# Performance work log

Measured on AMD Instinct MI355X. Metric: run time of the kernel, lower is better.

Reference implementation:

```python
import jax, jax.numpy as jnp
import numpy as np

N_HEADS = 12
EPS = 1e-6
H_DIM = 768


def setup_inputs() -> dict:
    key = jax.random.key(0)
    ks = jax.random.split(key, 10)
    B, M, T, C = 2, 64, 512, H_DIM
    x = jax.random.normal(ks[0], (B, M, T, C), dtype=jnp.float32)
    mask = jnp.ones((B, M, T), dtype=jnp.float32)
    s = 1.0 / np.sqrt(C)
    Wq = jax.random.normal(ks[1], (C, C), dtype=jnp.float32) * s
    bq = jax.random.normal(ks[2], (C,), dtype=jnp.float32) * 0.01
    Wk = jax.random.normal(ks[3], (C, C), dtype=jnp.float32) * s
    bk = jax.random.normal(ks[4], (C,), dtype=jnp.float32) * 0.01
    Wv = jax.random.normal(ks[5], (C, C), dtype=jnp.float32) * s
    bv = jax.random.normal(ks[6], (C,), dtype=jnp.float32) * 0.01
    Wp = jax.random.normal(ks[7], (C, C), dtype=jnp.float32) * s
    bp = jax.random.normal(ks[8], (C,), dtype=jnp.float32) * 0.01
    return {"x": x, "mask": mask, "Wq": Wq, "bq": bq, "Wk": Wk, "bk": bk,
            "Wv": Wv, "bv": bv, "Wp": Wp, "bp": bp}


def reference(x, mask, Wq, bq, Wk, bk, Wv, bv, Wp, bp):
    B, M, T, C = x.shape
    N, D = N_HEADS, C // N_HEADS
    # projections: nn.Linear -> x @ W.T + b, then [B,M,T,N,D] -> [B,M,N,T,D]
    q = (x @ Wq.T + bq).reshape(B, M, T, N, D).transpose(0, 1, 3, 2, 4)
    k = (x @ Wk.T + bk).reshape(B, M, T, N, D).transpose(0, 1, 3, 2, 4)
    v = (x @ Wv.T + bv).reshape(B, M, T, N, D).transpose(0, 1, 3, 2, 4)
    q = jax.nn.elu(q) + 1.0
    k = jax.nn.elu(k) + 1.0
    k = k * mask[:, :, None, :, None]
    # KtV[b,m,n,d,e] = sum_t k[b,m,n,t,d] * v[b,m,n,t,e]   (small [D,D] per head)
    KtV = jnp.einsum('bmntd,bmnte->bmnde', k, v)
    # Z[b,m,n,t] = 1 / (q . sum_t' k + eps)
    Z = 1.0 / (jnp.einsum('bmntd,bmnd->bmnt', q, k.sum(axis=-2)) + EPS)
    # torch code does Z.expand(...,T,D) @ KtV, which equals Z * KtV.sum(over d)
    S = KtV.sum(axis=-2)                       # [B,M,N,E]
    V = Z[..., None] * S[:, :, :, None, :]     # [B,M,N,T,E]
    V = V.transpose(0, 1, 3, 2, 4).reshape(B, M, T, N * D)
    out = V @ Wp.T + bp
    return out
```

## Files before the change

### kernel.cpp

```cpp
#include <hip/hip_runtime.h>
#include <hip/hip_bf16.h>
#include <stdint.h>

typedef short short8 __attribute__((ext_vector_type(8)));
typedef float f32x4 __attribute__((ext_vector_type(4)));

#define EPS_Z 1e-6f

__device__ __forceinline__ unsigned short f2bf(float f) {
  uint32_t b = __float_as_uint(f);
  b += 0x7FFFu + ((b >> 16) & 1u);
  return (unsigned short)(b >> 16);
}
__device__ __forceinline__ float bf2f(unsigned short u) {
  return __uint_as_float(((uint32_t)u) << 16);
}

__device__ __forceinline__ void gl16(const unsigned short* g, unsigned short* l) {
  __builtin_amdgcn_global_load_lds(
      (const __attribute__((address_space(1))) unsigned int*)g,
      (__attribute__((address_space(3))) unsigned int*)l, 16, 0, 0);
}

__global__ __launch_bounds__(256) void k_cvt(const float* __restrict__ in,
                                             unsigned short* __restrict__ out, int n) {
  int i = (blockIdx.x * 256 + threadIdx.x) * 8;
  if (i >= n) return;
  float4 a = *(const float4*)(in + i);
  float4 b = *(const float4*)(in + i + 4);
  union { unsigned short u[8]; short8 v; } r;
  r.u[0] = f2bf(a.x); r.u[1] = f2bf(a.y); r.u[2] = f2bf(a.z); r.u[3] = f2bf(a.w);
  r.u[4] = f2bf(b.x); r.u[5] = f2bf(b.y); r.u[6] = f2bf(b.z); r.u[7] = f2bf(b.w);
  *(short8*)(out + i) = r.v;
}

__global__ __launch_bounds__(512, 2) void k_projqk(
    const unsigned short* __restrict__ xbf,
    const unsigned short* __restrict__ Wkbf,
    const unsigned short* __restrict__ Wqbf,
    const float* __restrict__ bk,
    const float* __restrict__ bq,
    const float* __restrict__ mask,
    float* __restrict__ kd,
    float* __restrict__ ksum_part,
    unsigned short* __restrict__ qbf)
{
  __shared__ unsigned short Ab[128][64];
  __shared__ unsigned short Bkb[128][64];
  __shared__ unsigned short Bqb[128][64];
  __shared__ float rowf[128];
  __shared__ float kcol[2][128];

  const int tid = threadIdx.x;
  const int lane = tid & 63;
  const int wid = tid >> 6;
  const int isQ = wid >> 2;
  const int w2 = wid & 3;
  const int wr = w2 >> 1, wc = w2 & 1;
  const int colTile = blockIdx.x;
  const int rowTile = blockIdx.y;
  const int bm = rowTile >> 2;
  const int trow = rowTile & 3;
  const size_t rowBase = (size_t)rowTile * 128;
  const int colBase = colTile * 128;
  const int lrow = lane & 15;
  const int lgrp = lane >> 4;

  if (tid < 128) rowf[tid] = mask[bm * 512 + trow * 128 + tid];

  f32x4 acc[4][4] = {};

  for (int kt = 0; kt < 12; ++kt) {
    const int k0 = kt * 64;
    __syncthreads();
#pragma unroll
    for (int c = 0; c < 2; ++c) {
      const int chunk = c * 512 + tid;
      const int r = chunk >> 3;
      const int cc = chunk & 7;
      const int scc = cc ^ (r & 7);
      const int ldst = c * 4096 + wid * 512;
      gl16(xbf + (rowBase + r) * 768 + k0 + scc * 8, &Ab[0][0] + ldst);
      gl16(Wkbf + (size_t)(colBase + r) * 768 + k0 + scc * 8, &Bkb[0][0] + ldst);
      gl16(Wqbf + (size_t)(colBase + r) * 768 + k0 + scc * 8, &Bqb[0][0] + ldst);
    }
    __syncthreads();
    const unsigned short* Bsel = isQ ? &Bqb[0][0] : &Bkb[0][0];
#pragma unroll
    for (int kk = 0; kk < 64; kk += 32) {
      short8 av[4], bv4[4];
#pragma unroll
      for (int rf = 0; rf < 4; ++rf) {
        const int row = wr * 64 + rf * 16 + lrow;
        const int cidx = ((kk >> 3) + lgrp) ^ (row & 7);
        av[rf] = *(const short8*)&Ab[row][cidx * 8];
      }
#pragma unroll
      for (int cf = 0; cf < 4; ++cf) {
        const int row = wc * 64 + cf * 16 + lrow;
        const int cidx = ((kk >> 3) + lgrp) ^ (row & 7);
        bv4[cf] = *(const short8*)(Bsel + row * 64 + cidx * 8);
      }
#pragma unroll
      for (int rf = 0; rf < 4; ++rf)
#pragma unroll
        for (int cf = 0; cf < 4; ++cf)
          acc[rf][cf] = __builtin_amdgcn_mfma_f32_16x16x32_bf16(
              av[rf], bv4[cf], acc[rf][cf], 0, 0, 0);
    }
  }

  const float* bias = isQ ? bq : bk;
  float bvv[4];
#pragma unroll
  for (int cf = 0; cf < 4; ++cf)
    bvv[cf] = bias[colBase + wc * 64 + cf * 16 + lrow];
#pragma unroll
  for (int rf = 0; rf < 4; ++rf)
#pragma unroll
    for (int cf = 0; cf < 4; ++cf)
#pragma unroll
      for (int j = 0; j < 4; ++j) {
        float v = acc[rf][cf][j] + bvv[cf];
        v = (v > 0.0f) ? (v + 1.0f) : __expf(v);
        if (!isQ) v *= rowf[wr * 64 + rf * 16 + lgrp * 4 + j];
        acc[rf][cf][j] = v;
      }

  const int head = colTile * 2 + wc;

  if (!isQ) {
#pragma unroll
    for (int rf = 0; rf < 4; ++rf)
#pragma unroll
      for (int j = 0; j < 4; ++j) {
        float s = acc[rf][0][j] + acc[rf][1][j] + acc[rf][2][j] + acc[rf][3][j];
        s += __shfl_xor(s, 1, 64);
        s += __shfl_xor(s, 2, 64);
        s += __shfl_xor(s, 4, 64);
        s += __shfl_xor(s, 8, 64);
        if ((lane & 15) == 0) {
          const int t = trow * 128 + wr * 64 + rf * 16 + lgrp * 4 + j;
          kd[((size_t)bm * 512 + t) * 12 + head] = s;
        }
      }
#pragma unroll
    for (int cf = 0; cf < 4; ++cf) {
      float s = 0.f;
#pragma unroll
      for (int rf = 0; rf < 4; ++rf)
#pragma unroll
        for (int j = 0; j < 4; ++j) s += acc[rf][cf][j];
      s += __shfl_xor(s, 16, 64);
      s += __shfl_xor(s, 32, 64);
      if (lane < 16) kcol[wr][wc * 64 + cf * 16 + lane] = s;
    }
  } else {
#pragma unroll
    for (int rf = 0; rf < 4; ++rf)
#pragma unroll
      for (int j = 0; j < 4; ++j) {
        const int t = trow * 128 + wr * 64 + rf * 16 + lgrp * 4 + j;
        unsigned short* qp = qbf + (((size_t)bm * 12 + head) * 512 + t) * 64 + lrow;
#pragma unroll
        for (int cf = 0; cf < 4; ++cf)
          qp[cf * 16] = f2bf(acc[rf][cf][j]);
      }
  }

  __syncthreads();
  if (tid < 128)
    ksum_part[((size_t)bm * 4 + trow) * 768 + colBase + tid] =
        kcol[0][tid] + kcol[1][tid];
}

__global__ __launch_bounds__(192) void k_xk(const unsigned short* __restrict__ xbf,
                                            const float* __restrict__ kd,
                                            float* __restrict__ xk_part) {
  __shared__ float kdl[128][12];
  const int bm = blockIdx.x, ts = blockIdx.y, tid = threadIdx.x;
  for (int i = tid; i < 128 * 12; i += 192)
    kdl[i / 12][i % 12] = kd[((size_t)bm * 512 + ts * 128 + i / 12) * 12 + (i % 12)];
  __syncthreads();
  float a[12][4];
#pragma unroll
  for (int n = 0; n < 12; ++n)
#pragma unroll
    for (int j = 0; j < 4; ++j) a[n][j] = 0.f;
  const int c = tid * 4;
  const unsigned short* xp = xbf + ((size_t)bm * 512 + ts * 128) * 768 + c;
  for (int t = 0; t < 128; ++t) {
    ushort4 xv = *(const ushort4*)(xp + (size_t)t * 768);
    const float x0 = bf2f(xv.x), x1 = bf2f(xv.y), x2 = bf2f(xv.z), x3 = bf2f(xv.w);
#pragma unroll
    for (int n = 0; n < 12; ++n) {
      const float kv = kdl[t][n];
      a[n][0] += kv * x0; a[n][1] += kv * x1; a[n][2] += kv * x2; a[n][3] += kv * x3;
    }
  }
  float* op = xk_part + ((size_t)bm * 4 + ts) * 12 * 768 + c;
#pragma unroll
  for (int n = 0; n < 12; ++n)
    *(float4*)(op + (size_t)n * 768) = make_float4(a[n][0], a[n][1], a[n][2], a[n][3]);
}

__global__ __launch_bounds__(256) void k_sg(const float* __restrict__ ksum_part,
                                            const float* __restrict__ xk_part,
                                            const float* __restrict__ Wv,
                                            const float* __restrict__ bv,
                                            const float* __restrict__ Wp,
                                            float* __restrict__ G) {
  __shared__ __align__(16) float xk_l[768];
  __shared__ __align__(16) float S_l[64];
  __shared__ float kdsum_s;
  const int bm = blockIdx.x, n = blockIdx.y, tid = threadIdx.x;

  if (tid < 192) {
    const float* xp = xk_part + (size_t)bm * 4 * 9216 + n * 768 + tid * 4;
    float4 a = *(const float4*)(xp);
    float4 b = *(const float4*)(xp + 9216);
    float4 c = *(const float4*)(xp + 18432);
    float4 d = *(const float4*)(xp + 27648);
    *(float4*)&xk_l[tid * 4] = make_float4(a.x + b.x + c.x + d.x,
                                           a.y + b.y + c.y + d.y,
                                           a.z + b.z + c.z + d.z,
                                           a.w + b.w + c.w + d.w);
  } else {
    const int d = tid - 192;
    const float* kp = ksum_part + (size_t)bm * 4 * 768 + n * 64 + d;
    float s = kp[0] + kp[768] + kp[1536] + kp[2304];
    s += __shfl_xor(s, 1, 64);
    s += __shfl_xor(s, 2, 64);
    s += __shfl_xor(s, 4, 64);
    s += __shfl_xor(s, 8, 64);
    s += __shfl_xor(s, 16, 64);
    s += __shfl_xor(s, 32, 64);
    if (d == 0) kdsum_s = s;
  }
  __syncthreads();

  {
    const int e = tid >> 2, q = tid & 3;
    const float4* wv = (const float4*)(Wv + (size_t)(n * 64 + e) * 768 + q * 192);
    const float4* xp4 = (const float4*)(xk_l + q * 192);
    float s = 0.f;
#pragma unroll
    for (int i = 0; i < 48; ++i) {
      float4 w = wv[i], xx = xp4[i];
      s += w.x * xx.x + w.y * xx.y + w.z * xx.z + w.w * xx.w;
    }
    s += __shfl_xor(s, 1, 64);
    s += __shfl_xor(s, 2, 64);
    if (q == 0) S_l[e] = s + bv[n * 64 + e] * kdsum_s;
  }
  __syncthreads();

#pragma unroll
  for (int r = 0; r < 3; ++r) {
    const int p = r * 256 + tid;
    const float4* wp = (const float4*)(Wp + (size_t)p * 768 + n * 64);
    const float4* sp = (const float4*)S_l;
    float g = 0.f;
#pragma unroll
    for (int i = 0; i < 16; ++i) {
      float4 w = wp[i], s = sp[i];
      g += w.x * s.x + w.y * s.y + w.z * s.z + w.w * s.w;
    }
    G[((size_t)bm * 12 + n) * 768 + p] = g;
  }
}

__global__ __launch_bounds__(256) void k_z(const unsigned short* __restrict__ qbf,
                                           const float* __restrict__ ksum_part,
                                           float* __restrict__ Z) {
  __shared__ float ksum_l[768];
  const int bm = blockIdx.x, ts = blockIdx.y, tid = threadIdx.x;
  for (int i = tid; i < 768; i += 256) {
    const float* kp = ksum_part + (size_t)bm * 3072 + i;
    ksum_l[i] = kp[0] + kp[768] + kp[1536] + kp[2304];
  }
  __syncthreads();
#pragma unroll
  for (int i = 0; i < 6; ++i) {
    const int task = i * 256 + tid;
    const int n = task >> 7;
    const int t = ts * 128 + (task & 127);
    const unsigned short* qp = qbf + (((size_t)bm * 12 + n) * 512 + t) * 64;
    const float* kp = &ksum_l[n * 64];
    float s = 0.f;
#pragma unroll
    for (int c = 0; c < 8; ++c) {
      short8 qv = *(const short8*)(qp + c * 8);
      s += bf2f((unsigned short)qv[0]) * kp[c * 8 + 0]
         + bf2f((unsigned short)qv[1]) * kp[c * 8 + 1]
         + bf2f((unsigned short)qv[2]) * kp[c * 8 + 2]
         + bf2f((unsigned short)qv[3]) * kp[c * 8 + 3]
         + bf2f((unsigned short)qv[4]) * kp[c * 8 + 4]
         + bf2f((unsigned short)qv[5]) * kp[c * 8 + 5]
         + bf2f((unsigned short)qv[6]) * kp[c * 8 + 6]
         + bf2f((unsigned short)qv[7]) * kp[c * 8 + 7];
    }
    Z[((size_t)bm * 12 + n) * 512 + t] = 1.0f / (s + EPS_Z);
  }
}

__global__ __launch_bounds__(256) void k_out(const float* __restrict__ Z,
                                             const float* __restrict__ G,
                                             const float* __restrict__ bp,
                                             float* __restrict__ outp) {
  __shared__ __align__(16) float G_l[9216];
  __shared__ float Z_l[768];
  __shared__ __align__(16) float bp_l[768];
  const int bm = blockIdx.x;
  const int tbase = blockIdx.y * 64;
  const int tid = threadIdx.x;
  for (int i = tid; i < 9216; i += 256) G_l[i] = G[(size_t)bm * 9216 + i];
  for (int i = tid; i < 768; i += 256) {
    bp_l[i] = bp[i];
    Z_l[i] = Z[((size_t)bm * 12 + (i >> 6)) * 512 + tbase + (i & 63)];
  }
  __syncthreads();
  for (int it = 0; it < 48; ++it) {
    const int idx = it * 1024 + tid * 4;
    const int t = idx / 768;
    const int p = idx - t * 768;
    float4 o = *(const float4*)&bp_l[p];
#pragma unroll
    for (int n = 0; n < 12; ++n) {
      const float z = Z_l[n * 64 + t];
      const float4 g = *(const float4*)&G_l[n * 768 + p];
      o.x += z * g.x; o.y += z * g.y; o.z += z * g.z; o.w += z * g.w;
    }
    *(float4*)&outp[((size_t)bm * 512 + tbase + t) * 768 + p] = o;
  }
}

extern "C" void kernel_launch(void* const* d_in, const int* in_sizes, int n_in,
                              void* d_out, int out_size, void* d_ws, size_t ws_size,
                              hipStream_t stream) {
  const float* x    = (const float*)d_in[0];
  const float* mask = (const float*)d_in[1];
  const float* Wq   = (const float*)d_in[2];
  const float* bq   = (const float*)d_in[3];
  const float* Wk   = (const float*)d_in[4];
  const float* bk   = (const float*)d_in[5];
  const float* Wv   = (const float*)d_in[6];
  const float* bv   = (const float*)d_in[7];
  const float* Wp   = (const float*)d_in[8];
  const float* bp   = (const float*)d_in[9];
  float* outp = (float*)d_out;

  char* ws = (char*)d_ws;
  unsigned short* xbf  = (unsigned short*)(ws);
  unsigned short* Wkbf = (unsigned short*)(ws + 100663296);
  unsigned short* Wqbf = (unsigned short*)(ws + 101842944);
  float* kd        = (float*)(ws + 103022592);
  float* ksum_part = (float*)(ws + 106168320);
  float* xk_part   = (float*)(ws + 107741184);
  float* Zb        = (float*)(ws + 126615552);
  float* G         = (float*)(ws + 129761280);
  unsigned short* qbf = (unsigned short*)d_out;

  hipLaunchKernelGGL(k_cvt, dim3(24576), dim3(256), 0, stream, x, xbf, 50331648);
  hipLaunchKernelGGL(k_cvt, dim3(288), dim3(256), 0, stream, Wk, Wkbf, 589824);
  hipLaunchKernelGGL(k_cvt, dim3(288), dim3(256), 0, stream, Wq, Wqbf, 589824);
  hipLaunchKernelGGL(k_projqk, dim3(6, 512), dim3(512), 0, stream,
                     xbf, Wkbf, Wqbf, bk, bq, mask, kd, ksum_part, qbf);
  hipLaunchKernelGGL(k_xk, dim3(128, 4), dim3(192), 0, stream, xbf, kd, xk_part);
  hipLaunchKernelGGL(k_sg, dim3(128, 12), dim3(256), 0, stream,
                     ksum_part, xk_part, Wv, bv, Wp, G);
  hipLaunchKernelGGL(k_z, dim3(128, 4), dim3(256), 0, stream, qbf, ksum_part, Zb);
  hipLaunchKernelGGL(k_out, dim3(128, 8), dim3(256), 0, stream, Zb, G, bp, outp);
}
```

Before: 494.2 us.

## Merge conversion launches, swizzle projection grid, and fuse xk with Z kernel

```diff
diff --git a/kernel.cpp b/kernel.cpp
--- a/kernel.cpp
+++ b/kernel.cpp
@@ -22,10 +22,18 @@
       (__attribute__((address_space(3))) unsigned int*)l, 16, 0, 0);
 }
 
-__global__ __launch_bounds__(256) void k_cvt(const float* __restrict__ in,
-                                             unsigned short* __restrict__ out, int n) {
-  int i = (blockIdx.x * 256 + threadIdx.x) * 8;
-  if (i >= n) return;
+__global__ __launch_bounds__(256) void k_cvt_all(
+    const float* __restrict__ x, const float* __restrict__ Wk,
+    const float* __restrict__ Wq, unsigned short* __restrict__ xbf,
+    unsigned short* __restrict__ Wkbf, unsigned short* __restrict__ Wqbf) {
+  const int bid = blockIdx.x;
+  const float* in;
+  unsigned short* out;
+  int base;
+  if (bid < 24576)      { in = x;  out = xbf;  base = bid; }
+  else if (bid < 24864) { in = Wk; out = Wkbf; base = bid - 24576; }
+  else                  { in = Wq; out = Wqbf; base = bid - 24864; }
+  const int i = (base * 256 + threadIdx.x) * 8;
   float4 a = *(const float4*)(in + i);
   float4 b = *(const float4*)(in + i + 4);
   union { unsigned short u[8]; short8 v; } r;
@@ -57,8 +65,10 @@
   const int isQ = wid >> 2;
   const int w2 = wid & 3;
   const int wr = w2 >> 1, wc = w2 & 1;
-  const int colTile = blockIdx.x;
-  const int rowTile = blockIdx.y;
+  const int flat = blockIdx.x;
+  const int swz = (flat & 7) * 384 + (flat >> 3);
+  const int colTile = swz % 6;
+  const int rowTile = swz / 6;
   const int bm = rowTile >> 2;
   const int trow = rowTile & 3;
   const size_t rowBase = (size_t)rowTile * 128;
@@ -174,34 +184,73 @@
         kcol[0][tid] + kcol[1][tid];
 }
 
-__global__ __launch_bounds__(192) void k_xk(const unsigned short* __restrict__ xbf,
-                                            const float* __restrict__ kd,
-                                            float* __restrict__ xk_part) {
-  __shared__ float kdl[128][12];
-  const int bm = blockIdx.x, ts = blockIdx.y, tid = threadIdx.x;
-  for (int i = tid; i < 128 * 12; i += 192)
-    kdl[i / 12][i % 12] = kd[((size_t)bm * 512 + ts * 128 + i / 12) * 12 + (i % 12)];
-  __syncthreads();
-  float a[12][4];
-#pragma unroll
-  for (int n = 0; n < 12; ++n)
-#pragma unroll
-    for (int j = 0; j < 4; ++j) a[n][j] = 0.f;
-  const int c = tid * 4;
-  const unsigned short* xp = xbf + ((size_t)bm * 512 + ts * 128) * 768 + c;
-  for (int t = 0; t < 128; ++t) {
-    ushort4 xv = *(const ushort4*)(xp + (size_t)t * 768);
-    const float x0 = bf2f(xv.x), x1 = bf2f(xv.y), x2 = bf2f(xv.z), x3 = bf2f(xv.w);
-#pragma unroll
-    for (int n = 0; n < 12; ++n) {
-      const float kv = kdl[t][n];
-      a[n][0] += kv * x0; a[n][1] += kv * x1; a[n][2] += kv * x2; a[n][3] += kv * x3;
-    }
-  }
-  float* op = xk_part + ((size_t)bm * 4 + ts) * 12 * 768 + c;
-#pragma unroll
-  for (int n = 0; n < 12; ++n)
-    *(float4*)(op + (size_t)n * 768) = make_float4(a[n][0], a[n][1], a[n][2], a[n][3]);
+__global__ __launch_bounds__(256) void k_xkz(const unsigned short* __restrict__ xbf,
+                                             const float* __restrict__ kd,
+                                             float* __restrict__ xk_part,
+                                             const unsigned short* __restrict__ qbf,
+                                             const float* __restrict__ ksum_part,
+                                             float* __restrict__ Z) {
+  const int bid = blockIdx.x, tid = threadIdx.x;
+  if (bid < 512) {
+    __shared__ float kdl[128][12];
+    const int bm = bid >> 2, ts = bid & 3;
+    for (int i = tid; i < 128 * 12; i += 256)
+      kdl[i / 12][i % 12] = kd[((size_t)bm * 512 + ts * 128 + i / 12) * 12 + (i % 12)];
+    __syncthreads();
+    if (tid < 192) {
+      float a[12][4];
+#pragma unroll
+      for (int n = 0; n < 12; ++n)
+#pragma unroll
+        for (int j = 0; j < 4; ++j) a[n][j] = 0.f;
+      const int c = tid * 4;
+      const unsigned short* xp = xbf + ((size_t)bm * 512 + ts * 128) * 768 + c;
+      for (int t = 0; t < 128; ++t) {
+        ushort4 xv = *(const ushort4*)(xp + (size_t)t * 768);
+        const float x0 = bf2f(xv.x), x1 = bf2f(xv.y), x2 = bf2f(xv.z), x3 = bf2f(xv.w);
+#pragma unroll
+        for (int n = 0; n < 12; ++n) {
+          const float kv = kdl[t][n];
+          a[n][0] += kv * x0; a[n][1] += kv * x1; a[n][2] += kv * x2; a[n][3] += kv * x3;
+        }
+      }
+      float* op = xk_part + ((size_t)bm * 4 + ts) * 12 * 768 + c;
+#pragma unroll
+      for (int n = 0; n < 12; ++n)
+        *(float4*)(op + (size_t)n * 768) = make_float4(a[n][0], a[n][1], a[n][2], a[n][3]);
+    }
+  } else {
+    __shared__ float ksum_l[768];
+    const int b2 = bid - 512;
+    const int bm = b2 >> 2, ts = b2 & 3;
+    for (int i = tid; i < 768; i += 256) {
+      const float* kp = ksum_part + (size_t)bm * 3072 + i;
+      ksum_l[i] = kp[0] + kp[768] + kp[1536] + kp[2304];
+    }
+    __syncthreads();
+#pragma unroll
+    for (int i = 0; i < 6; ++i) {
+      const int task = i * 256 + tid;
+      const int n = task >> 7;
+      const int t = ts * 128 + (task & 127);
+      const unsigned short* qp = qbf + (((size_t)bm * 12 + n) * 512 + t) * 64;
+      const float* kp = &ksum_l[n * 64];
+      float s = 0.f;
+#pragma unroll
+      for (int c = 0; c < 8; ++c) {
+        short8 qv = *(const short8*)(qp + c * 8);
+        s += bf2f((unsigned short)qv[0]) * kp[c * 8 + 0]
+           + bf2f((unsigned short)qv[1]) * kp[c * 8 + 1]
+           + bf2f((unsigned short)qv[2]) * kp[c * 8 + 2]
+           + bf2f((unsigned short)qv[3]) * kp[c * 8 + 3]
+           + bf2f((unsigned short)qv[4]) * kp[c * 8 + 4]
+           + bf2f((unsigned short)qv[5]) * kp[c * 8 + 5]
+           + bf2f((unsigned short)qv[6]) * kp[c * 8 + 6]
+           + bf2f((unsigned short)qv[7]) * kp[c * 8 + 7];
+      }
+      Z[((size_t)bm * 12 + n) * 512 + t] = 1.0f / (s + EPS_Z);
+    }
+  }
 }
 
 __global__ __launch_bounds__(256) void k_sg(const float* __restrict__ ksum_part,
@@ -270,40 +319,6 @@
   }
 }
 
-__global__ __launch_bounds__(256) void k_z(const unsigned short* __restrict__ qbf,
-                                           const float* __restrict__ ksum_part,
-                                           float* __restrict__ Z) {
-  __shared__ float ksum_l[768];
-  const int bm = blockIdx.x, ts = blockIdx.y, tid = threadIdx.x;
-  for (int i = tid; i < 768; i += 256) {
-    const float* kp = ksum_part + (size_t)bm * 3072 + i;
-    ksum_l[i] = kp[0] + kp[768] + kp[1536] + kp[2304];
-  }
-  __syncthreads();
-#pragma unroll
-  for (int i = 0; i < 6; ++i) {
-    const int task = i * 256 + tid;
-    const int n = task >> 7;
-    const int t = ts * 128 + (task & 127);
-    const unsigned short* qp = qbf + (((size_t)bm * 12 + n) * 512 + t) * 64;
-    const float* kp = &ksum_l[n * 64];
-    float s = 0.f;
-#pragma unroll
-    for (int c = 0; c < 8; ++c) {
-      short8 qv = *(const short8*)(qp + c * 8);
-      s += bf2f((unsigned short)qv[0]) * kp[c * 8 + 0]
-         + bf2f((unsigned short)qv[1]) * kp[c * 8 + 1]
-         + bf2f((unsigned short)qv[2]) * kp[c * 8 + 2]
-         + bf2f((unsigned short)qv[3]) * kp[c * 8 + 3]
-         + bf2f((unsigned short)qv[4]) * kp[c * 8 + 4]
-         + bf2f((unsigned short)qv[5]) * kp[c * 8 + 5]
-         + bf2f((unsigned short)qv[6]) * kp[c * 8 + 6]
-         + bf2f((unsigned short)qv[7]) * kp[c * 8 + 7];
-    }
-    Z[((size_t)bm * 12 + n) * 512 + t] = 1.0f / (s + EPS_Z);
-  }
-}
-
 __global__ __launch_bounds__(256) void k_out(const float* __restrict__ Z,
                                              const float* __restrict__ G,
                                              const float* __restrict__ bp,
@@ -361,14 +376,13 @@
   float* G         = (float*)(ws + 129761280);
   unsigned short* qbf = (unsigned short*)d_out;
 
-  hipLaunchKernelGGL(k_cvt, dim3(24576), dim3(256), 0, stream, x, xbf, 50331648);
-  hipLaunchKernelGGL(k_cvt, dim3(288), dim3(256), 0, stream, Wk, Wkbf, 589824);
-  hipLaunchKernelGGL(k_cvt, dim3(288), dim3(256), 0, stream, Wq, Wqbf, 589824);
-  hipLaunchKernelGGL(k_projqk, dim3(6, 512), dim3(512), 0, stream,
+  hipLaunchKernelGGL(k_cvt_all, dim3(25152), dim3(256), 0, stream,
+                     x, Wk, Wq, xbf, Wkbf, Wqbf);
+  hipLaunchKernelGGL(k_projqk, dim3(3072), dim3(512), 0, stream,
                      xbf, Wkbf, Wqbf, bk, bq, mask, kd, ksum_part, qbf);
-  hipLaunchKernelGGL(k_xk, dim3(128, 4), dim3(192), 0, stream, xbf, kd, xk_part);
+  hipLaunchKernelGGL(k_xkz, dim3(1024), dim3(256), 0, stream,
+                     xbf, kd, xk_part, qbf, ksum_part, Zb);
   hipLaunchKernelGGL(k_sg, dim3(128, 12), dim3(256), 0, stream,
                      ksum_part, xk_part, Wv, bv, Wp, G);
-  hipLaunchKernelGGL(k_z, dim3(128, 4), dim3(256), 0, stream, qbf, ksum_part, Zb);
   hipLaunchKernelGGL(k_out, dim3(128, 8), dim3(256), 0, stream, Zb, G, bp, outp);
 }
```

Result: faster. 481.6 us (-2.6%).
